# Kernel optimization log

Measured on AMD Instinct MI355X. Metric: run time of the kernel, lower is better.

Reference implementation:

```python
import jax, jax.numpy as jnp
import numpy as np

B, T, D, M = 32, 2048, 128, 256   # batch, seq_len, pitch vocab d, encoder_output_dim m
FILTERS = [256, 256, 256]
TAU = 1.0                          # gumbel_temperature
ALPHA_INV = 1.0 / (D * 100)        # W init value: 1/alpha, alpha = d*100


def causal_dilated_conv(x, w, b, dilation):
    """x: [B,T,Cin], w: [K,Cin,Cout], causal left padding."""
    k = w.shape[0]
    pad = (k - 1) * dilation
    y = jax.lax.conv_general_dilated(
        x, w, window_strides=(1,), padding=[(pad, 0)],
        rhs_dilation=(dilation,),
        dimension_numbers=('NWC', 'WIO', 'NWC'))
    return y + b


def slow_weight_model(batch, w0, b0, w1, b1, w2, b2, w_out, b_out):
    """DilatedConvBlock: stack of causal dilated convs (relu) + 1x1 readout to m logits."""
    h = jax.nn.relu(causal_dilated_conv(batch, w0, b0, dilation=1))
    h = jax.nn.relu(causal_dilated_conv(h, w1, b1, dilation=2))
    h = jax.nn.relu(causal_dilated_conv(h, w2, b2, dilation=4))
    return causal_dilated_conv(h, w_out, b_out, dilation=1)  # [B,T,M] logits


def setup_inputs() -> dict:
    key = jax.random.key(0)
    ks = jax.random.split(key, 9)
    def glorot(k, shape):
        fan_in = np.prod(shape[:-1])
        return (jax.random.normal(k, shape, jnp.float32) / np.sqrt(fan_in)).astype(jnp.float32)
    return {
        'batch': jax.random.uniform(ks[0], (B, T, D), jnp.float32),
        'w0': glorot(ks[1], (2, D, FILTERS[0])), 'b0': jnp.zeros((FILTERS[0],), jnp.float32),
        'w1': glorot(ks[2], (2, FILTERS[0], FILTERS[1])), 'b1': jnp.zeros((FILTERS[1],), jnp.float32),
        'w2': glorot(ks[3], (2, FILTERS[1], FILTERS[2])), 'b2': jnp.zeros((FILTERS[2],), jnp.float32),
        'w_out': glorot(ks[4], (1, FILTERS[2], M)), 'b_out': jnp.zeros((M,), jnp.float32),
    }


def reference(batch, w0, b0, w1, b1, w2, b2, w_out, b_out):
    logits = slow_weight_model(batch, w0, b0, w1, b1, w2, b2, w_out, b_out)  # [B,T,M]
    # short_term_method == 'softmax_normalize_after'
    h_src = jax.nn.softmax(logits / TAU, axis=2)  # [B,T,M]
    s_tar = batch                                  # [B,T,D]
    W0 = jnp.full((B, M, D), ALPHA_INV, jnp.float32)

    def step(W, hs):
        h, s = hs                                              # [B,M], [B,D]
        num = jnp.einsum('bm,bmd->bd', h, W)                   # readout
        prob = num / jnp.sum(num, axis=-1, keepdims=True)      # normalize-after
        W_new = W + h[:, :, None] * s[:, None, :]              # outer-product fast-weight update
        return W_new, prob

    W_final, probs = jax.lax.scan(
        step, W0, (jnp.swapaxes(h_src, 0, 1), jnp.swapaxes(s_tar, 0, 1)))
    probs = jnp.swapaxes(probs, 0, 1)  # [B,T,D]
    return probs, W_final
```

## Files before the change

### kernel.cpp

```cpp
#include <hip/hip_runtime.h>

using u16 = unsigned short;
using u32 = unsigned int;
using short8 = __attribute__((ext_vector_type(8))) short;
using short4v = __attribute__((ext_vector_type(4))) short;
using bf16x8 = __attribute__((ext_vector_type(8))) __bf16;
using f32x4 = __attribute__((ext_vector_type(4))) float;

#define ALPHA_INV (1.0f / (128.0f * 100.0f))

__device__ __forceinline__ u32 swz(u32 off, u32 row) { return off ^ ((row & 7u) << 4); }

__device__ __forceinline__ u16 f2bf(float x) {
  u32 u = __float_as_uint(x);
  u32 r = u + 0x7fffu + ((u >> 16) & 1u);
  return (u16)(r >> 16);
}

__device__ __forceinline__ float bf2f(u16 x) {
  u32 u = ((u32)x) << 16;
  return __uint_as_float(u);
}

__device__ __forceinline__ f32x4 mfma(bf16x8 a, bf16x8 b, f32x4 c) {
  return __builtin_amdgcn_mfma_f32_16x16x32_bf16(a, b, c, 0, 0, 0);
}

__device__ __forceinline__ void gl16(const void* g, void* l) {
  __builtin_amdgcn_global_load_lds(
      (const __attribute__((address_space(1))) unsigned int*)g,
      (__attribute__((address_space(3))) unsigned int*)l, 16, 0, 0);
}

__global__ void wtrans(const float* __restrict__ w, u16* __restrict__ o, int rows, int cin) {
  int idx = blockIdx.x * 256 + threadIdx.x;
  if (idx >= rows * 256) return;
  int row = idx >> 8, n = idx & 255;
  int tap = row / cin, c = row - tap * cin;
  int kc = c >> 6, ci = c & 63;
  u32 sb = (u32)(ci * 2) ^ ((u32)(n & 7) << 4);
  o[((size_t)tap * 256 + n) * cin + kc * 64 + (sb >> 1)] = f2bf(w[idx]);
}

__global__ void cvt_bf16_kernel(const float* __restrict__ in, u16* __restrict__ out) {
  int i = blockIdx.x * 256 + threadIdx.x;
  float4 v = ((const float4*)in)[i];
  short4v o;
  o[0] = (short)f2bf(v.x); o[1] = (short)f2bf(v.y);
  o[2] = (short)f2bf(v.z); o[3] = (short)f2bf(v.w);
  int e = i * 4;
  int row = e >> 7, c = e & 127;
  int slice = c >> 6, ci = c & 63;
  u32 sb = (u32)(ci * 2) ^ ((u32)(row & 7) << 4);
  *(short4v*)(out + (size_t)row * 128 + slice * 64 + (sb >> 1)) = o;
}

__global__ __launch_bounds__(256) void transpose_s(const u16* __restrict__ S,
                                                   u16* __restrict__ ST) {
  __shared__ u16 L[64 * 129];
  const int tid = threadIdx.x;
  const int t0 = blockIdx.x * 64;
  const int b = blockIdx.y;
  const u16* src = S + ((size_t)b * 2048 + t0) * 128;
#pragma unroll
  for (int it = 0; it < 4; ++it) {
    int s = tid + it * 256;
    int t = s >> 4, c8 = s & 15;
    int slice = c8 >> 3;
    u32 sb = (u32)((c8 & 7) * 16) ^ ((u32)(t & 7) << 4);
    short8 v = *(const short8*)(src + t * 128 + slice * 64 + (sb >> 1));
#pragma unroll
    for (int j = 0; j < 8; ++j) L[t * 129 + c8 * 8 + j] = (u16)v[j];
  }
  __syncthreads();
  u16* dst = ST + (size_t)b * 128 * 2048 + t0;
#pragma unroll
  for (int it = 0; it < 4; ++it) {
    int s = tid + it * 256;
    int oct = s & 7, d = s >> 3;
    short8 v;
#pragma unroll
    for (int j = 0; j < 8; ++j) v[j] = (short)L[(oct * 8 + j) * 129 + d];
    *(short8*)(dst + (size_t)d * 2048 + oct * 8) = v;
  }
}

template <int CIN, int DIL, int TAPS, bool RELU, bool SOFTMAX>
__global__ __launch_bounds__(512) void conv_kernel(
    const u16* __restrict__ in, const u16* __restrict__ wt,
    const float* __restrict__ bias, u16* __restrict__ out) {
  constexpr int BM = 128, BN = 256, BK = 64;
  __shared__ alignas(16) u16 Al[BM * BK];
  __shared__ alignas(16) u16 Bl[BN * BK];
  __shared__ float redA[4][BM];
  __shared__ float redB[4][BM];

  const int tid = threadIdx.x;
  const int wid = tid >> 6, lane = tid & 63;
  const int wr = wid >> 2, wc = wid & 3;
  const int lg = lane >> 4, lq = lane & 15;
  const int row0 = blockIdx.x * BM;
  const int tloc0 = row0 & 2047;

  f32x4 acc[4][4];
#pragma unroll
  for (int i = 0; i < 4; ++i)
#pragma unroll
    for (int j = 0; j < 4; ++j) acc[i][j] = (f32x4)0.0f;

#pragma unroll
  for (int tap = 0; tap < TAPS; ++tap) {
    const int shift = (TAPS - 1 - tap) * DIL;
#pragma unroll
    for (int kc = 0; kc < CIN / BK; ++kc) {
      if (shift > 0 && tloc0 == 0) {
#pragma unroll
        for (int it = 0; it < 2; ++it) {
          int gi = tid + it * 512;
          int r = gi >> 3, cg = gi & 7;
          short8 v = (short8)0;
          if (r >= shift)
            v = *(const short8*)(in + (size_t)(row0 + r - shift) * CIN + kc * BK + cg * 8);
          *(short8*)((char*)Al + gi * 16) = v;
        }
      } else {
#pragma unroll
        for (int it = 0; it < 2; ++it) {
          int gi = tid + it * 512;
          int r = gi >> 3, cg = gi & 7;
          gl16(in + (size_t)(row0 + r - shift) * CIN + kc * BK + cg * 8,
               (char*)Al + it * 8192 + wid * 1024);
        }
      }
      {
        const u16* wtb = wt + ((size_t)(tap * 256)) * CIN + kc * BK;
#pragma unroll
        for (int it = 0; it < 4; ++it) {
          int gi = tid + it * 512;
          int n = gi >> 3, cg = gi & 7;
          gl16(wtb + (size_t)n * CIN + cg * 8, (char*)Bl + it * 8192 + wid * 1024);
        }
      }
      __syncthreads();
#pragma unroll
      for (int ks = 0; ks < 2; ++ks) {
        bf16x8 af[4], bfr[4];
#pragma unroll
        for (int mi = 0; mi < 4; ++mi) {
          int r = wr * 64 + mi * 16 + lq;
          af[mi] = *(const bf16x8*)((const char*)Al +
                                    swz(r * 128 + ks * 64 + lg * 16, (u32)(r - shift + 8)));
        }
#pragma unroll
        for (int ni = 0; ni < 4; ++ni) {
          int n = wc * 64 + ni * 16 + lq;
          bfr[ni] = *(const bf16x8*)((const char*)Bl + swz(n * 128 + ks * 64 + lg * 16, n));
        }
#pragma unroll
        for (int mi = 0; mi < 4; ++mi)
#pragma unroll
          for (int ni = 0; ni < 4; ++ni)
            acc[mi][ni] = mfma(af[mi], bfr[ni], acc[mi][ni]);
      }
      __syncthreads();
    }
  }

  float bcol[4];
#pragma unroll
  for (int ni = 0; ni < 4; ++ni) bcol[ni] = bias[wc * 64 + ni * 16 + lq];
#pragma unroll
  for (int mi = 0; mi < 4; ++mi)
#pragma unroll
    for (int ni = 0; ni < 4; ++ni)
#pragma unroll
      for (int rr = 0; rr < 4; ++rr) acc[mi][ni][rr] += bcol[ni];

  if constexpr (!SOFTMAX) {
#pragma unroll
    for (int mi = 0; mi < 4; ++mi)
#pragma unroll
      for (int ni = 0; ni < 4; ++ni)
#pragma unroll
        for (int rr = 0; rr < 4; ++rr) {
          float v = acc[mi][ni][rr];
          if (RELU) v = fmaxf(v, 0.0f);
          int row = row0 + wr * 64 + mi * 16 + lg * 4 + rr;
          int col = wc * 64 + ni * 16 + lq;
          int ci = col & 63;
          u32 sb = (u32)(ci * 2) ^ ((u32)(row & 7) << 4);
          out[(size_t)row * BN + wc * 64 + (sb >> 1)] = f2bf(v);
        }
  } else {
    float tmx[4][4];
#pragma unroll
    for (int mi = 0; mi < 4; ++mi)
#pragma unroll
      for (int rr = 0; rr < 4; ++rr) {
        float v = fmaxf(fmaxf(acc[mi][0][rr], acc[mi][1][rr]),
                        fmaxf(acc[mi][2][rr], acc[mi][3][rr]));
#pragma unroll
        for (int off = 1; off < 16; off <<= 1) v = fmaxf(v, __shfl_xor(v, off));
        if (lq == 0) redA[wc][wr * 64 + mi * 16 + lg * 4 + rr] = v;
      }
    __syncthreads();
#pragma unroll
    for (int mi = 0; mi < 4; ++mi)
#pragma unroll
      for (int rr = 0; rr < 4; ++rr) {
        int rb = wr * 64 + mi * 16 + lg * 4 + rr;
        tmx[mi][rr] = fmaxf(fmaxf(redA[0][rb], redA[1][rb]),
                            fmaxf(redA[2][rb], redA[3][rb]));
      }
#pragma unroll
    for (int mi = 0; mi < 4; ++mi)
#pragma unroll
      for (int rr = 0; rr < 4; ++rr) {
        float s = 0.0f;
#pragma unroll
        for (int ni = 0; ni < 4; ++ni) {
          float p = __expf(acc[mi][ni][rr] - tmx[mi][rr]);
          acc[mi][ni][rr] = p;
          s += p;
        }
#pragma unroll
        for (int off = 1; off < 16; off <<= 1) s += __shfl_xor(s, off);
        if (lq == 0) redB[wc][wr * 64 + mi * 16 + lg * 4 + rr] = s;
      }
    __syncthreads();
#pragma unroll
    for (int mi = 0; mi < 4; ++mi)
#pragma unroll
      for (int rr = 0; rr < 4; ++rr) {
        int rb = wr * 64 + mi * 16 + lg * 4 + rr;
        float inv = 1.0f / (redB[0][rb] + redB[1][rb] + redB[2][rb] + redB[3][rb]);
        int row = row0 + rb;
#pragma unroll
        for (int ni = 0; ni < 4; ++ni) {
          int col = wc * 64 + ni * 16 + lq;
          out[(size_t)row * BN + col] = f2bf(acc[mi][ni][rr] * inv);
        }
      }
  }
}

__global__ __launch_bounds__(512) void gchunk(
    const u16* __restrict__ H, const u16* __restrict__ ST,
    u16* __restrict__ G0, u16* __restrict__ G1) {
  constexpr int M = 256, T = 2048;
  __shared__ alignas(16) u16 Hl[128 * 128];
  __shared__ alignas(16) u16 Sl[128 * 128];
  const int tid = threadIdx.x;
  const int wid = tid >> 6, lane = tid & 63;
  const int dg = wid >> 2, mg = wid & 3;
  const int lg = lane >> 4, lq = lane & 15;
  const int b = blockIdx.x, mh = blockIdx.y, j = blockIdx.z;
  u16* G = (mh == 0 ? G0 : G1);

#pragma unroll
  for (int it = 0; it < 4; ++it) {
    int s = tid + it * 512;
    int t = s >> 4, c8 = s & 15;
    *(short8*)((char*)Hl + swz(t * 256 + c8 * 16, t)) =
        *(const short8*)(H + ((size_t)b * T + j * 128 + t) * M + mh * 128 + c8 * 8);
  }
#pragma unroll
  for (int it = 0; it < 4; ++it) {
    int s = tid + it * 512;
    int d = s >> 4, c8 = s & 15;
    *(short8*)((char*)Sl + swz(d * 256 + c8 * 16, d)) =
        *(const short8*)(ST + ((size_t)b * 128 + d) * T + j * 128 + c8 * 8);
  }
  __syncthreads();

  f32x4 acc[4][2];
#pragma unroll
  for (int di = 0; di < 4; ++di)
#pragma unroll
    for (int mi = 0; mi < 2; ++mi) acc[di][mi] = (f32x4)0.0f;

#pragma unroll
  for (int ks = 0; ks < 4; ++ks) {
    bf16x8 sfrag[4];
#pragma unroll
    for (int di = 0; di < 4; ++di) {
      int d = dg * 64 + di * 16 + lq;
      sfrag[di] = *(const bf16x8*)((const char*)Sl + swz(d * 256 + ks * 64 + lg * 16, d));
    }
#pragma unroll
    for (int mi = 0; mi < 2; ++mi) {
      int ml = mg * 32 + mi * 16 + lq;
      short8 hr;
#pragma unroll
      for (int jj = 0; jj < 8; ++jj) {
        int t = ks * 32 + lg * 8 + jj;
        hr[jj] = (short)*(const u16*)((const char*)Hl + swz(t * 256 + ml * 2, t));
      }
      bf16x8 hfrag = __builtin_bit_cast(bf16x8, hr);
#pragma unroll
      for (int di = 0; di < 4; ++di) acc[di][mi] = mfma(sfrag[di], hfrag, acc[di][mi]);
    }
  }

  u16* Gj = G + (((size_t)b * 16 + j) << 14);
#pragma unroll
  for (int di = 0; di < 4; ++di)
#pragma unroll
    for (int mi = 0; mi < 2; ++mi)
#pragma unroll
      for (int rr = 0; rr < 4; ++rr) {
        int d = dg * 64 + di * 16 + lg * 4 + rr;
        int ml = mg * 32 + mi * 16 + lq;
        Gj[d * 128 + ml] = f2bf(acc[di][mi][rr]);
      }
}

__global__ __launch_bounds__(256) void prefix_scan(
    u16* __restrict__ G0, u16* __restrict__ G1, float* __restrict__ Wtmp) {
  u16* G = blockIdx.y ? G1 : G0;
  float* W = Wtmp + (size_t)blockIdx.y * (32 * 128 * 128);
  int idx = blockIdx.x * 256 + threadIdx.x;
  int mo = idx & 15, d = (idx >> 4) & 127, b = idx >> 11;
  size_t base = (((size_t)b * 16) * 128 + d) * 128 + mo * 8;
  float acc[8];
#pragma unroll
  for (int k = 0; k < 8; ++k) acc[k] = ALPHA_INV;
  for (int j = 0; j < 16; ++j) {
    u16* p = G + base + (size_t)j * 16384;
    short8 g = *(short8*)p;
    short8 c;
#pragma unroll
    for (int k = 0; k < 8; ++k) c[k] = (short)f2bf(acc[k]);
    *(short8*)p = c;
#pragma unroll
    for (int k = 0; k < 8; ++k) acc[k] += bf2f((u16)g[k]);
  }
  float* w = W + ((size_t)b * 128 + d) * 128 + mo * 8;
  *(float4*)w = make_float4(acc[0], acc[1], acc[2], acc[3]);
  *(float4*)(w + 4) = make_float4(acc[4], acc[5], acc[6], acc[7]);
}

__global__ __launch_bounds__(256) void wfin_t(const float* __restrict__ Wtmp,
                                              float* __restrict__ wfin) {
  __shared__ float L[128 * 129];
  const int tid = threadIdx.x;
  const int b = blockIdx.x, h = blockIdx.y;
  const float* src = Wtmp + (size_t)h * (32 * 128 * 128) + (size_t)b * 16384;
#pragma unroll
  for (int it = 0; it < 16; ++it) {
    int idx = tid + it * 256;
    int d = idx >> 5, q = idx & 31;
    *(float4*)&L[d * 129 + q * 4] = *(const float4*)&src[d * 128 + q * 4];
  }
  __syncthreads();
  float* dst = wfin + (size_t)b * 32768 + (size_t)h * 16384;
#pragma unroll
  for (int it = 0; it < 16; ++it) {
    int idx = tid + it * 256;
    int ml = idx >> 5, dq = idx & 31;
    float4 v;
    v.x = L[(dq * 4 + 0) * 129 + ml];
    v.y = L[(dq * 4 + 1) * 129 + ml];
    v.z = L[(dq * 4 + 2) * 129 + ml];
    v.w = L[(dq * 4 + 3) * 129 + ml];
    *(float4*)&dst[ml * 128 + dq * 4] = v;
  }
}

__global__ __launch_bounds__(512) void attn_chunk(
    const u16* __restrict__ H, const u16* __restrict__ ST,
    const u16* __restrict__ C0, const u16* __restrict__ C1,
    float* __restrict__ out) {
  constexpr int M = 256, D = 128, T = 2048;
  __shared__ alignas(16) u16 Hi[128 * 256];
  __shared__ alignas(16) u16 Sl[128 * 128];
  __shared__ alignas(16) u16 Ct[128 * 128];

  const int tid = threadIdx.x;
  const int wid = tid >> 6, lane = tid & 63;
  const int lg = lane >> 4, lq = lane & 15;
  const int b = blockIdx.x, i = blockIdx.y;
  const size_t hrow0 = (size_t)b * T + i * 128;

  bf16x8 aq[8];
  {
    const u16* qrow = H + (hrow0 + wid * 16 + lq) * M;
#pragma unroll
    for (int ks = 0; ks < 8; ++ks) aq[ks] = *(const bf16x8*)(qrow + ks * 32 + lg * 8);
  }

#pragma unroll
  for (int it = 0; it < 8; ++it) {
    int s = tid + it * 512;
    int r = s >> 5, c = s & 31;
    *(short8*)((char*)Hi + swz(r * 512 + c * 16, r)) =
        *(const short8*)(H + (hrow0 + r) * M + c * 8);
  }
#pragma unroll
  for (int it = 0; it < 4; ++it) {
    int s = tid + it * 512;
    int d = s >> 4, c8 = s & 15;
    *(short8*)((char*)Sl + swz(d * 256 + c8 * 16, d)) =
        *(const short8*)(ST + ((size_t)b * D + d) * T + i * 128 + c8 * 8);
  }
  const size_t coff = ((size_t)b * 16 + i) * (128 * 128);
#pragma unroll
  for (int it = 0; it < 4; ++it) {
    int s = tid + it * 512;
    int d = s >> 4, c8 = s & 15;
    *(short8*)((char*)Ct + swz(d * 256 + c8 * 16, d)) = *(const short8*)(C0 + coff + d * 128 + c8 * 8);
  }
  __syncthreads();

  f32x4 accO[8];
#pragma unroll
  for (int df = 0; df < 8; ++df) accO[df] = (f32x4)0.0f;

#pragma unroll
  for (int ks = 0; ks < 4; ++ks)
#pragma unroll
    for (int df = 0; df < 8; ++df) {
      int d = df * 16 + lq;
      bf16x8 bf = *(const bf16x8*)((const char*)Ct + swz(d * 256 + ks * 64 + lg * 16, d));
      accO[df] = mfma(aq[ks], bf, accO[df]);
    }
  __syncthreads();
#pragma unroll
  for (int it = 0; it < 4; ++it) {
    int s = tid + it * 512;
    int d = s >> 4, c8 = s & 15;
    *(short8*)((char*)Ct + swz(d * 256 + c8 * 16, d)) = *(const short8*)(C1 + coff + d * 128 + c8 * 8);
  }
  __syncthreads();
#pragma unroll
  for (int ks = 0; ks < 4; ++ks)
#pragma unroll
    for (int df = 0; df < 8; ++df) {
      int d = df * 16 + lq;
      bf16x8 bf = *(const bf16x8*)((const char*)Ct + swz(d * 256 + ks * 64 + lg * 16, d));
      accO[df] = mfma(aq[4 + ks], bf, accO[df]);
    }
  __syncthreads();

  f32x4 accP[8];
#pragma unroll
  for (int cf = 0; cf < 8; ++cf) accP[cf] = (f32x4)0.0f;
#pragma unroll
  for (int ks = 0; ks < 8; ++ks)
#pragma unroll
    for (int cf = 0; cf < 8; ++cf) {
      int tt = cf * 16 + lq;
      bf16x8 bf = *(const bf16x8*)((const char*)Hi + swz(tt * 512 + ks * 64 + lg * 16, tt));
      accP[cf] = mfma(aq[ks], bf, accP[cf]);
    }
  char* Pw = (char*)Ct + wid * 4096;
#pragma unroll
  for (int cf = 0; cf < 8; ++cf)
#pragma unroll
    for (int rr = 0; rr < 4; ++rr) {
      int ql = lg * 4 + rr;
      int tl = cf * 16 + lq;
      float v = accP[cf][rr];
      if (tl >= wid * 16 + ql) v = 0.0f;
      *(u16*)(Pw + swz(ql * 256 + tl * 2, ql)) = f2bf(v);
    }
#pragma unroll
  for (int ks = 0; ks < 4; ++ks) {
    bf16x8 a = *(const bf16x8*)(Pw + swz(lq * 256 + ks * 64 + lg * 16, lq));
#pragma unroll
    for (int df = 0; df < 8; ++df) {
      int d = df * 16 + lq;
      bf16x8 bf = *(const bf16x8*)((const char*)Sl + swz(d * 256 + ks * 64 + lg * 16, d));
      accO[df] = mfma(a, bf, accO[df]);
    }
  }

#pragma unroll
  for (int rr = 0; rr < 4; ++rr) {
    float ssum = 0.0f;
#pragma unroll
    for (int df = 0; df < 8; ++df) ssum += accO[df][rr];
#pragma unroll
    for (int off = 1; off < 16; off <<= 1) ssum += __shfl_xor(ssum, off);
    float inv = 1.0f / ssum;
    size_t row = hrow0 + wid * 16 + lg * 4 + rr;
#pragma unroll
    for (int df = 0; df < 8; ++df)
      out[row * D + df * 16 + lq] = accO[df][rr] * inv;
  }
}

extern "C" void kernel_launch(void* const* d_in, const int* in_sizes, int n_in,
                              void* d_out, int out_size, void* d_ws, size_t ws_size,
                              hipStream_t stream) {
  const float* batch = (const float*)d_in[0];
  const float* w0 = (const float*)d_in[1];
  const float* b0 = (const float*)d_in[2];
  const float* w1 = (const float*)d_in[3];
  const float* b1 = (const float*)d_in[4];
  const float* w2 = (const float*)d_in[5];
  const float* b2 = (const float*)d_in[6];
  const float* wo = (const float*)d_in[7];
  const float* bo = (const float*)d_in[8];

  const size_t SZ_S = 16777216;
  const size_t SZ_BUF = 33554432;
  const size_t NEED = SZ_S + 2 * SZ_BUF + 786432;
  if (ws_size < NEED) return;

  char* ws = (char*)d_ws;
  u16* S = (u16*)ws;
  u16* bufA = (u16*)(ws + SZ_S);
  u16* bufB = (u16*)(ws + SZ_S + SZ_BUF);
  u16* Wt0 = (u16*)(ws + SZ_S + 2 * SZ_BUF);
  u16* Wt1 = Wt0 + 2 * 256 * 128;
  u16* Wt2 = Wt1 + 2 * 256 * 256;
  u16* Wt3 = Wt2 + 2 * 256 * 256;
  u16* ST = bufA;
  u16* G0 = (u16*)ws;
  u16* G1 = (u16*)(ws + 2 * SZ_S);
  float* probs = (float*)d_out;
  float* wfin = probs + (size_t)32 * 2048 * 128;
  float* Wtmp = probs;

  wtrans<<<256, 256, 0, stream>>>(w0, Wt0, 2 * 128, 128);
  wtrans<<<512, 256, 0, stream>>>(w1, Wt1, 2 * 256, 256);
  wtrans<<<512, 256, 0, stream>>>(w2, Wt2, 2 * 256, 256);
  wtrans<<<256, 256, 0, stream>>>(wo, Wt3, 1 * 256, 256);
  cvt_bf16_kernel<<<8192, 256, 0, stream>>>(batch, S);

  conv_kernel<128, 1, 2, true, false><<<512, 512, 0, stream>>>(S, Wt0, b0, bufA);
  conv_kernel<256, 2, 2, true, false><<<512, 512, 0, stream>>>(bufA, Wt1, b1, bufB);
  conv_kernel<256, 4, 2, true, false><<<512, 512, 0, stream>>>(bufB, Wt2, b2, bufA);
  conv_kernel<256, 1, 1, false, true><<<512, 512, 0, stream>>>(bufA, Wt3, bo, bufB);

  transpose_s<<<dim3(32, 32), 256, 0, stream>>>(S, ST);
  gchunk<<<dim3(32, 2, 16), 512, 0, stream>>>(bufB, ST, G0, G1);
  prefix_scan<<<dim3(256, 2), 256, 0, stream>>>(G0, G1, Wtmp);
  wfin_t<<<dim3(32, 2), 256, 0, stream>>>(Wtmp, wfin);
  attn_chunk<<<dim3(32, 16), 512, 0, stream>>>(bufB, ST, G0, G1, probs);
}
```

Before: 204.8 us.

## Merge weight transposes, fuse prefix scan with final-W transpose, transpose H in LDS

Folds the four weight-conversion launches into one kernel, and fuses the chunk prefix scan with the final W transpose so the fp32 temporary round-trip through the output buffer goes away. In gchunk, H is now stored transposed in LDS so each MFMA operand is a single 16-byte LDS read instead of eight scalar reads. In attn_chunk, the second correction chunk is prefetched into registers early to hide its global load latency. The gchunk change trades scalar 2-byte LDS stores for the vector reads, and the prefetch adds register pressure.

```diff
diff --git a/kernel.cpp b/kernel.cpp
--- a/kernel.cpp
+++ b/kernel.cpp
@@ -32,9 +32,17 @@
       (__attribute__((address_space(3))) unsigned int*)l, 16, 0, 0);
 }
 
-__global__ void wtrans(const float* __restrict__ w, u16* __restrict__ o, int rows, int cin) {
-  int idx = blockIdx.x * 256 + threadIdx.x;
-  if (idx >= rows * 256) return;
+__global__ void wtrans_all(const float* __restrict__ w0, const float* __restrict__ w1,
+                           const float* __restrict__ w2, const float* __restrict__ wo,
+                           u16* __restrict__ o0, u16* __restrict__ o1,
+                           u16* __restrict__ o2, u16* __restrict__ o3) {
+  int blk = blockIdx.x;
+  const float* w; u16* o; int cin;
+  if (blk < 256)       { w = w0; o = o0; cin = 128; }
+  else if (blk < 768)  { w = w1; o = o1; cin = 256; blk -= 256; }
+  else if (blk < 1280) { w = w2; o = o2; cin = 256; blk -= 768; }
+  else                 { w = wo; o = o3; cin = 256; blk -= 1280; }
+  int idx = blk * 256 + threadIdx.x;
   int row = idx >> 8, n = idx & 255;
   int tap = row / cin, c = row - tap * cin;
   int kc = c >> 6, ci = c & 63;
@@ -261,8 +269,12 @@
   for (int it = 0; it < 4; ++it) {
     int s = tid + it * 512;
     int t = s >> 4, c8 = s & 15;
-    *(short8*)((char*)Hl + swz(t * 256 + c8 * 16, t)) =
-        *(const short8*)(H + ((size_t)b * T + j * 128 + t) * M + mh * 128 + c8 * 8);
+    short8 v = *(const short8*)(H + ((size_t)b * T + j * 128 + t) * M + mh * 128 + c8 * 8);
+#pragma unroll
+    for (int jj = 0; jj < 8; ++jj) {
+      int ml = c8 * 8 + jj;
+      *(u16*)((char*)Hl + swz(ml * 256 + t * 2, ml)) = (u16)v[jj];
+    }
   }
 #pragma unroll
   for (int it = 0; it < 4; ++it) {
@@ -290,13 +302,8 @@
 #pragma unroll
     for (int mi = 0; mi < 2; ++mi) {
       int ml = mg * 32 + mi * 16 + lq;
-      short8 hr;
-#pragma unroll
-      for (int jj = 0; jj < 8; ++jj) {
-        int t = ks * 32 + lg * 8 + jj;
-        hr[jj] = (short)*(const u16*)((const char*)Hl + swz(t * 256 + ml * 2, t));
-      }
-      bf16x8 hfrag = __builtin_bit_cast(bf16x8, hr);
+      bf16x8 hfrag =
+          *(const bf16x8*)((const char*)Hl + swz(ml * 256 + ks * 64 + lg * 16, ml));
 #pragma unroll
       for (int di = 0; di < 4; ++di) acc[di][mi] = mfma(sfrag[di], hfrag, acc[di][mi]);
     }
@@ -315,18 +322,20 @@
       }
 }
 
-__global__ __launch_bounds__(256) void prefix_scan(
-    u16* __restrict__ G0, u16* __restrict__ G1, float* __restrict__ Wtmp) {
-  u16* G = blockIdx.y ? G1 : G0;
-  float* W = Wtmp + (size_t)blockIdx.y * (32 * 128 * 128);
-  int idx = blockIdx.x * 256 + threadIdx.x;
-  int mo = idx & 15, d = (idx >> 4) & 127, b = idx >> 11;
-  size_t base = (((size_t)b * 16) * 128 + d) * 128 + mo * 8;
+__global__ __launch_bounds__(256) void prefix_wfin(
+    u16* __restrict__ G0, u16* __restrict__ G1, float* __restrict__ wfin) {
+  __shared__ float Wl[16][132];
+  const int b = blockIdx.x, mh = blockIdx.y, ds = blockIdx.z;
+  u16* G = mh ? G1 : G0;
+  const int tid = threadIdx.x;
+  const int mo = tid & 15, dg = tid >> 4;
+  const int d = ds * 16 + dg;
+  size_t base = (((size_t)b * 16) << 14) + d * 128 + mo * 8;
   float acc[8];
 #pragma unroll
   for (int k = 0; k < 8; ++k) acc[k] = ALPHA_INV;
   for (int j = 0; j < 16; ++j) {
-    u16* p = G + base + (size_t)j * 16384;
+    u16* p = G + base + ((size_t)j << 14);
     short8 g = *(short8*)p;
     short8 c;
 #pragma unroll
@@ -335,36 +344,16 @@
 #pragma unroll
     for (int k = 0; k < 8; ++k) acc[k] += bf2f((u16)g[k]);
   }
-  float* w = W + ((size_t)b * 128 + d) * 128 + mo * 8;
-  *(float4*)w = make_float4(acc[0], acc[1], acc[2], acc[3]);
-  *(float4*)(w + 4) = make_float4(acc[4], acc[5], acc[6], acc[7]);
-}
-
-__global__ __launch_bounds__(256) void wfin_t(const float* __restrict__ Wtmp,
-                                              float* __restrict__ wfin) {
-  __shared__ float L[128 * 129];
-  const int tid = threadIdx.x;
-  const int b = blockIdx.x, h = blockIdx.y;
-  const float* src = Wtmp + (size_t)h * (32 * 128 * 128) + (size_t)b * 16384;
-#pragma unroll
-  for (int it = 0; it < 16; ++it) {
-    int idx = tid + it * 256;
-    int d = idx >> 5, q = idx & 31;
-    *(float4*)&L[d * 129 + q * 4] = *(const float4*)&src[d * 128 + q * 4];
-  }
-  __syncthreads();
-  float* dst = wfin + (size_t)b * 32768 + (size_t)h * 16384;
-#pragma unroll
-  for (int it = 0; it < 16; ++it) {
-    int idx = tid + it * 256;
-    int ml = idx >> 5, dq = idx & 31;
-    float4 v;
-    v.x = L[(dq * 4 + 0) * 129 + ml];
-    v.y = L[(dq * 4 + 1) * 129 + ml];
-    v.z = L[(dq * 4 + 2) * 129 + ml];
-    v.w = L[(dq * 4 + 3) * 129 + ml];
-    *(float4*)&dst[ml * 128 + dq * 4] = v;
-  }
+#pragma unroll
+  for (int k = 0; k < 8; ++k) Wl[dg][mo * 8 + k] = acc[k];
+  __syncthreads();
+  const int ml = tid >> 1, dq = tid & 1;
+  const int dl0 = dq * 8;
+  float* dst = wfin + ((size_t)b * 256 + mh * 128 + ml) * 128 + ds * 16 + dl0;
+  float4 v0 = make_float4(Wl[dl0][ml], Wl[dl0 + 1][ml], Wl[dl0 + 2][ml], Wl[dl0 + 3][ml]);
+  float4 v1 = make_float4(Wl[dl0 + 4][ml], Wl[dl0 + 5][ml], Wl[dl0 + 6][ml], Wl[dl0 + 7][ml]);
+  *(float4*)dst = v0;
+  *(float4*)(dst + 4) = v1;
 }
 
 __global__ __launch_bounds__(512) void attn_chunk(
@@ -381,6 +370,7 @@
   const int lg = lane >> 4, lq = lane & 15;
   const int b = blockIdx.x, i = blockIdx.y;
   const size_t hrow0 = (size_t)b * T + i * 128;
+  const size_t coff = ((size_t)b * 16 + i) * (128 * 128);
 
   bf16x8 aq[8];
   {
@@ -389,6 +379,14 @@
     for (int ks = 0; ks < 8; ++ks) aq[ks] = *(const bf16x8*)(qrow + ks * 32 + lg * 8);
   }
 
+  short8 ct1r[4];
+#pragma unroll
+  for (int it = 0; it < 4; ++it) {
+    int s = tid + it * 512;
+    int d = s >> 4, c8 = s & 15;
+    ct1r[it] = *(const short8*)(C1 + coff + d * 128 + c8 * 8);
+  }
+
 #pragma unroll
   for (int it = 0; it < 8; ++it) {
     int s = tid + it * 512;
@@ -403,7 +401,6 @@
     *(short8*)((char*)Sl + swz(d * 256 + c8 * 16, d)) =
         *(const short8*)(ST + ((size_t)b * D + d) * T + i * 128 + c8 * 8);
   }
-  const size_t coff = ((size_t)b * 16 + i) * (128 * 128);
 #pragma unroll
   for (int it = 0; it < 4; ++it) {
     int s = tid + it * 512;
@@ -429,7 +426,7 @@
   for (int it = 0; it < 4; ++it) {
     int s = tid + it * 512;
     int d = s >> 4, c8 = s & 15;
-    *(short8*)((char*)Ct + swz(d * 256 + c8 * 16, d)) = *(const short8*)(C1 + coff + d * 128 + c8 * 8);
+    *(short8*)((char*)Ct + swz(d * 256 + c8 * 16, d)) = ct1r[it];
   }
   __syncthreads();
 #pragma unroll
@@ -521,12 +518,8 @@
   u16* G1 = (u16*)(ws + 2 * SZ_S);
   float* probs = (float*)d_out;
   float* wfin = probs + (size_t)32 * 2048 * 128;
-  float* Wtmp = probs;
-
-  wtrans<<<256, 256, 0, stream>>>(w0, Wt0, 2 * 128, 128);
-  wtrans<<<512, 256, 0, stream>>>(w1, Wt1, 2 * 256, 256);
-  wtrans<<<512, 256, 0, stream>>>(w2, Wt2, 2 * 256, 256);
-  wtrans<<<256, 256, 0, stream>>>(wo, Wt3, 1 * 256, 256);
+
+  wtrans_all<<<1536, 256, 0, stream>>>(w0, w1, w2, wo, Wt0, Wt1, Wt2, Wt3);
   cvt_bf16_kernel<<<8192, 256, 0, stream>>>(batch, S);
 
   conv_kernel<128, 1, 2, true, false><<<512, 512, 0, stream>>>(S, Wt0, b0, bufA);
@@ -536,7 +529,6 @@
 
   transpose_s<<<dim3(32, 32), 256, 0, stream>>>(S, ST);
   gchunk<<<dim3(32, 2, 16), 512, 0, stream>>>(bufB, ST, G0, G1);
-  prefix_scan<<<dim3(256, 2), 256, 0, stream>>>(G0, G1, Wtmp);
-  wfin_t<<<dim3(32, 2), 256, 0, stream>>>(Wtmp, wfin);
+  prefix_wfin<<<dim3(32, 2, 8), 256, 0, stream>>>(G0, G1, wfin);
   attn_chunk<<<dim3(32, 16), 512, 0, stream>>>(bufB, ST, G0, G1, probs);
 }
```

New measurement: 200.1 us. 1.02x faster.
